# Performance work log

Measured on AMD Instinct MI355X. Metric: run time of the kernel, lower is better.

## Reference

```python
import jax, jax.numpy as jnp
import numpy as np

N, C, H, W = 64, 384, 56, 56   # local feature map
M, D = 16, 384                  # global tokens, d_model


def setup_inputs() -> dict:
    key = jax.random.key(0)
    k0, k1, k2, k3 = jax.random.split(key, 4)
    local_feature = jax.random.normal(k0, (N, C, H, W), dtype=jnp.float32)
    x = jax.random.normal(k1, (N, M, D), dtype=jnp.float32)
    # nn.Linear params: weight [out, in], bias [out]
    Wq = jax.random.normal(k2, (C, D), dtype=jnp.float32) * (1.0 / np.sqrt(D))
    bq = jnp.zeros((C,), dtype=jnp.float32)
    Wu = jax.random.normal(k3, (D, C), dtype=jnp.float32) * (1.0 / np.sqrt(C))
    bu = jnp.zeros((D,), dtype=jnp.float32)
    return {"local_feature": local_feature, "x": x, "Wq": Wq, "bq": bq, "Wu": Wu, "bu": bu}


def reference(local_feature, x, Wq, bq, Wu, bu):
    n, c, h, w = local_feature.shape
    # n c h w -> n (h w) c
    lf = local_feature.reshape(n, c, h * w).transpose(0, 2, 1)  # [n, L, c]
    q = x @ Wq.T + bq                                           # [n, M, c]
    scores = jnp.einsum('nmc,nlc->nml', q, lf) * (c ** -0.5)    # [n, M, L]
    attn = jax.nn.softmax(scores, axis=-1)
    fusion = jnp.einsum('nml,nlc->nmc', attn, lf)               # [n, M, c]
    return fusion @ Wu.T + bu + x                               # residual to x
```

## Files before the change

kernel.cpp:

```cpp
#include <hip/hip_runtime.h>
#include <math.h>

#define N_ 64
#define C_ 384
#define L_ 3136
#define M_ 16
#define D_ 384

__global__ __launch_bounds__(128) void k1_qproj(const float* __restrict__ x,
                                                const float* __restrict__ Wq,
                                                const float* __restrict__ bq,
                                                float* __restrict__ qs) {
    const int n = blockIdx.x;
    const int c = blockIdx.y * 128 + threadIdx.x;
    const float4* __restrict__ wrow = (const float4*)(Wq + (size_t)c * D_);
    const float4* __restrict__ xn   = (const float4*)(x + (size_t)n * M_ * D_);
    float acc[M_];
#pragma unroll
    for (int m = 0; m < M_; ++m) acc[m] = 0.f;
    for (int dq = 0; dq < D_ / 4; ++dq) {
        const float4 wv = wrow[dq];
#pragma unroll
        for (int m = 0; m < M_; ++m) {
            const float4 xv = xn[m * (D_ / 4) + dq];
            acc[m] += wv.x * xv.x + wv.y * xv.y + wv.z * xv.z + wv.w * xv.w;
        }
    }
    const float rs = 0.05103103630798287f;
    const float b = bq[c];
    float* qout = qs + ((size_t)n * C_ + c) * M_;
#pragma unroll
    for (int m = 0; m < M_; ++m) qout[m] = (acc[m] + b) * rs;
}

__global__ __launch_bounds__(256) void k2_scores(const float* __restrict__ lf,
                                                 const float* __restrict__ qs,
                                                 float* __restrict__ scores) {
    const int n = blockIdx.x;
    const int s = blockIdx.y;
    const int t = threadIdx.x;
    const bool active = (t < 224);
    const int l0 = s * 448 + (active ? t : 0) * 2;
    const float* __restrict__ lfn = lf + (size_t)n * C_ * L_;
    const float* __restrict__ qn  = qs + (size_t)n * C_ * M_;
    float accx[M_], accy[M_];
#pragma unroll
    for (int m = 0; m < M_; ++m) { accx[m] = 0.f; accy[m] = 0.f; }
    if (active) {
#pragma unroll 4
        for (int c = 0; c < C_; ++c) {
            const float2 lv = *(const float2*)(lfn + (size_t)c * L_ + l0);
            const float* __restrict__ qv = qn + c * M_;
#pragma unroll
            for (int m = 0; m < M_; ++m) {
                accx[m] += qv[m] * lv.x;
                accy[m] += qv[m] * lv.y;
            }
        }
        float* sn = scores + (size_t)n * M_ * L_;
#pragma unroll
        for (int m = 0; m < M_; ++m) {
            *(float2*)(sn + (size_t)m * L_ + l0) = make_float2(accx[m], accy[m]);
        }
    }
}

__global__ __launch_bounds__(64) void k3_softmax(float* __restrict__ scores) {
    float* row = scores + (size_t)blockIdx.x * L_;
    const int t = threadIdx.x;
    float lmax = -1e30f;
    for (int i = t; i < L_ / 4; i += 64) {
        const float4 v = ((const float4*)row)[i];
        lmax = fmaxf(lmax, fmaxf(fmaxf(v.x, v.y), fmaxf(v.z, v.w)));
    }
#pragma unroll
    for (int o = 32; o > 0; o >>= 1) lmax = fmaxf(lmax, __shfl_xor(lmax, o, 64));
    float lsum = 0.f;
    for (int i = t; i < L_ / 4; i += 64) {
        const float4 v = ((const float4*)row)[i];
        lsum += expf(v.x - lmax) + expf(v.y - lmax) +
                expf(v.z - lmax) + expf(v.w - lmax);
    }
#pragma unroll
    for (int o = 32; o > 0; o >>= 1) lsum += __shfl_xor(lsum, o, 64);
    const float inv = 1.0f / lsum;
    for (int i = t; i < L_ / 4; i += 64) {
        float4 v = ((const float4*)row)[i];
        v.x = expf(v.x - lmax) * inv;
        v.y = expf(v.y - lmax) * inv;
        v.z = expf(v.z - lmax) * inv;
        v.w = expf(v.w - lmax) * inv;
        ((float4*)row)[i] = v;
    }
}

__global__ __launch_bounds__(384) void k4_fusion(const float* __restrict__ lf,
                                                 const float* __restrict__ attn,
                                                 float* __restrict__ fusionP) {
    const int n = blockIdx.x;
    const int s = blockIdx.y;
    const int c = threadIdx.x;
    const float* __restrict__ lrow = lf + ((size_t)n * C_ + c) * L_;
    const float* __restrict__ an   = attn + (size_t)n * M_ * L_;
    float acc[M_];
#pragma unroll
    for (int m = 0; m < M_; ++m) acc[m] = 0.f;
    const int l0 = s * 392;
#pragma unroll 2
    for (int lq = 0; lq < 98; ++lq) {
        const int l = l0 + lq * 4;
        const float4 lv = *(const float4*)(lrow + l);
#pragma unroll
        for (int m = 0; m < M_; ++m) {
            const float4 av = *(const float4*)(an + (size_t)m * L_ + l);
            acc[m] += av.x * lv.x + av.y * lv.y + av.z * lv.z + av.w * lv.w;
        }
    }
    float* fp = fusionP + ((size_t)(n * 8 + s) * M_) * C_;
#pragma unroll
    for (int m = 0; m < M_; ++m) fp[m * C_ + c] = acc[m];
}

__global__ __launch_bounds__(256) void k4b_reduce(float* __restrict__ fusionP) {
    const int i = blockIdx.x * 256 + threadIdx.x;
    const int n = i / (M_ * C_);
    const int mc = i % (M_ * C_);
    float* p = fusionP + (size_t)n * 8 * M_ * C_ + mc;
    float v = p[0];
#pragma unroll
    for (int s2 = 1; s2 < 8; ++s2) v += p[s2 * M_ * C_];
    p[0] = v;
}

__global__ __launch_bounds__(128) void k5_out(const float* __restrict__ fusionP,
                                              const float* __restrict__ Wu,
                                              const float* __restrict__ bu,
                                              const float* __restrict__ x,
                                              float* __restrict__ out) {
    const int n = blockIdx.x;
    const int d = blockIdx.y * 128 + threadIdx.x;
    const float4* __restrict__ wrow = (const float4*)(Wu + (size_t)d * C_);
    const float4* __restrict__ fn   = (const float4*)(fusionP + (size_t)n * 8 * M_ * C_);
    float acc[M_];
#pragma unroll
    for (int m = 0; m < M_; ++m) acc[m] = 0.f;
    for (int cq = 0; cq < C_ / 4; ++cq) {
        const float4 wv = wrow[cq];
#pragma unroll
        for (int m = 0; m < M_; ++m) {
            const float4 fv = fn[m * (C_ / 4) + cq];
            acc[m] += wv.x * fv.x + wv.y * fv.y + wv.z * fv.z + wv.w * fv.w;
        }
    }
    const float b = bu[d];
#pragma unroll
    for (int m = 0; m < M_; ++m) {
        const size_t o = ((size_t)n * M_ + m) * D_ + d;
        out[o] = acc[m] + b + x[o];
    }
}

extern "C" void kernel_launch(void* const* d_in, const int* in_sizes, int n_in,
                              void* d_out, int out_size, void* d_ws, size_t ws_size,
                              hipStream_t stream) {
    const float* lf = (const float*)d_in[0];
    const float* x  = (const float*)d_in[1];
    const float* Wq = (const float*)d_in[2];
    const float* bq = (const float*)d_in[3];
    const float* Wu = (const float*)d_in[4];
    const float* bu = (const float*)d_in[5];
    float* out = (float*)d_out;

    float* ws      = (float*)d_ws;
    float* qs      = ws;
    float* scores  = qs + 393216;
    float* fusionP = scores + 3211264;

    k1_qproj  <<<dim3(64, 3), 128, 0, stream>>>(x, Wq, bq, qs);
    k2_scores <<<dim3(64, 7), 256, 0, stream>>>(lf, qs, scores);
    k3_softmax<<<1024, 64, 0, stream>>>(scores);
    k4_fusion <<<dim3(64, 8), 384, 0, stream>>>(lf, scores, fusionP);
    k4b_reduce<<<1536, 256, 0, stream>>>(fusionP);
    k5_out    <<<dim3(64, 3), 128, 0, stream>>>(fusionP, Wu, bu, x, out);
}
```

Baseline: 644.4 us.

## Fuse exp into scores, defer softmax normalization, tile fusion kernel through LDS

```diff
diff --git a/kernel.cpp b/kernel.cpp
--- a/kernel.cpp
+++ b/kernel.cpp
@@ -6,6 +6,7 @@
 #define L_ 3136
 #define M_ 16
 #define D_ 384
+#define SPL 49
 
 __global__ __launch_bounds__(128) void k1_qproj(const float* __restrict__ x,
                                                 const float* __restrict__ Wq,
@@ -33,114 +34,154 @@
     for (int m = 0; m < M_; ++m) qout[m] = (acc[m] + b) * rs;
 }
 
-__global__ __launch_bounds__(256) void k2_scores(const float* __restrict__ lf,
-                                                 const float* __restrict__ qs,
-                                                 float* __restrict__ scores) {
-    const int n = blockIdx.x;
-    const int s = blockIdx.y;
+__global__ __launch_bounds__(64) void k2_scores_exp(const float* __restrict__ lf,
+                                                    const float* __restrict__ qs,
+                                                    float* __restrict__ e_out,
+                                                    float* __restrict__ Sp) {
+    const int s = blockIdx.x;
+    const int n = blockIdx.y;
     const int t = threadIdx.x;
-    const bool active = (t < 224);
-    const int l0 = s * 448 + (active ? t : 0) * 2;
-    const float* __restrict__ lfn = lf + (size_t)n * C_ * L_;
+    const int l = s * 64 + t;
+    const float* __restrict__ lfn = lf + (size_t)n * C_ * L_ + l;
     const float* __restrict__ qn  = qs + (size_t)n * C_ * M_;
-    float accx[M_], accy[M_];
-#pragma unroll
-    for (int m = 0; m < M_; ++m) { accx[m] = 0.f; accy[m] = 0.f; }
-    if (active) {
-#pragma unroll 4
-        for (int c = 0; c < C_; ++c) {
-            const float2 lv = *(const float2*)(lfn + (size_t)c * L_ + l0);
-            const float* __restrict__ qv = qn + c * M_;
-#pragma unroll
-            for (int m = 0; m < M_; ++m) {
-                accx[m] += qv[m] * lv.x;
-                accy[m] += qv[m] * lv.y;
-            }
-        }
-        float* sn = scores + (size_t)n * M_ * L_;
-#pragma unroll
-        for (int m = 0; m < M_; ++m) {
-            *(float2*)(sn + (size_t)m * L_ + l0) = make_float2(accx[m], accy[m]);
-        }
-    }
-}
-
-__global__ __launch_bounds__(64) void k3_softmax(float* __restrict__ scores) {
-    float* row = scores + (size_t)blockIdx.x * L_;
-    const int t = threadIdx.x;
-    float lmax = -1e30f;
-    for (int i = t; i < L_ / 4; i += 64) {
-        const float4 v = ((const float4*)row)[i];
-        lmax = fmaxf(lmax, fmaxf(fmaxf(v.x, v.y), fmaxf(v.z, v.w)));
-    }
-#pragma unroll
-    for (int o = 32; o > 0; o >>= 1) lmax = fmaxf(lmax, __shfl_xor(lmax, o, 64));
-    float lsum = 0.f;
-    for (int i = t; i < L_ / 4; i += 64) {
-        const float4 v = ((const float4*)row)[i];
-        lsum += expf(v.x - lmax) + expf(v.y - lmax) +
-                expf(v.z - lmax) + expf(v.w - lmax);
-    }
-#pragma unroll
-    for (int o = 32; o > 0; o >>= 1) lsum += __shfl_xor(lsum, o, 64);
-    const float inv = 1.0f / lsum;
-    for (int i = t; i < L_ / 4; i += 64) {
-        float4 v = ((const float4*)row)[i];
-        v.x = expf(v.x - lmax) * inv;
-        v.y = expf(v.y - lmax) * inv;
-        v.z = expf(v.z - lmax) * inv;
-        v.w = expf(v.w - lmax) * inv;
-        ((float4*)row)[i] = v;
-    }
-}
-
-__global__ __launch_bounds__(384) void k4_fusion(const float* __restrict__ lf,
-                                                 const float* __restrict__ attn,
-                                                 float* __restrict__ fusionP) {
-    const int n = blockIdx.x;
-    const int s = blockIdx.y;
-    const int c = threadIdx.x;
-    const float* __restrict__ lrow = lf + ((size_t)n * C_ + c) * L_;
-    const float* __restrict__ an   = attn + (size_t)n * M_ * L_;
     float acc[M_];
 #pragma unroll
     for (int m = 0; m < M_; ++m) acc[m] = 0.f;
-    const int l0 = s * 392;
-#pragma unroll 2
-    for (int lq = 0; lq < 98; ++lq) {
-        const int l = l0 + lq * 4;
-        const float4 lv = *(const float4*)(lrow + l);
-#pragma unroll
-        for (int m = 0; m < M_; ++m) {
-            const float4 av = *(const float4*)(an + (size_t)m * L_ + l);
-            acc[m] += av.x * lv.x + av.y * lv.y + av.z * lv.z + av.w * lv.w;
-        }
-    }
-    float* fp = fusionP + ((size_t)(n * 8 + s) * M_) * C_;
-#pragma unroll
-    for (int m = 0; m < M_; ++m) fp[m * C_ + c] = acc[m];
-}
-
-__global__ __launch_bounds__(256) void k4b_reduce(float* __restrict__ fusionP) {
-    const int i = blockIdx.x * 256 + threadIdx.x;
-    const int n = i / (M_ * C_);
-    const int mc = i % (M_ * C_);
-    float* p = fusionP + (size_t)n * 8 * M_ * C_ + mc;
-    float v = p[0];
-#pragma unroll
-    for (int s2 = 1; s2 < 8; ++s2) v += p[s2 * M_ * C_];
-    p[0] = v;
-}
-
-__global__ __launch_bounds__(128) void k5_out(const float* __restrict__ fusionP,
+    for (int c = 0; c < C_; c += 8) {
+        float lv[8];
+#pragma unroll
+        for (int u = 0; u < 8; ++u) lv[u] = lfn[(size_t)(c + u) * L_];
+#pragma unroll
+        for (int u = 0; u < 8; ++u) {
+            const float lvu = lv[u];
+            const float4* __restrict__ qv = (const float4*)(qn + (size_t)(c + u) * M_);
+            const float4 q0 = qv[0], q1 = qv[1], q2 = qv[2], q3 = qv[3];
+            acc[0]  += q0.x * lvu; acc[1]  += q0.y * lvu; acc[2]  += q0.z * lvu; acc[3]  += q0.w * lvu;
+            acc[4]  += q1.x * lvu; acc[5]  += q1.y * lvu; acc[6]  += q1.z * lvu; acc[7]  += q1.w * lvu;
+            acc[8]  += q2.x * lvu; acc[9]  += q2.y * lvu; acc[10] += q2.z * lvu; acc[11] += q2.w * lvu;
+            acc[12] += q3.x * lvu; acc[13] += q3.y * lvu; acc[14] += q3.z * lvu; acc[15] += q3.w * lvu;
+        }
+    }
+    float e[M_];
+#pragma unroll
+    for (int m = 0; m < M_; ++m) e[m] = __expf(acc[m]);
+    float* __restrict__ eo = e_out + (size_t)n * M_ * L_ + l;
+#pragma unroll
+    for (int m = 0; m < M_; ++m) eo[(size_t)m * L_] = e[m];
+    float own = 0.f;
+#pragma unroll
+    for (int m = 0; m < M_; ++m) {
+        float v = e[m];
+#pragma unroll
+        for (int o = 32; o > 0; o >>= 1) v += __shfl_xor(v, o, 64);
+        if (t == m) own = v;
+    }
+    if (t < M_) Sp[((size_t)n * SPL + s) * M_ + t] = own;
+}
+
+__global__ __launch_bounds__(256) void k4_fusion(const float* __restrict__ lf,
+                                                 const float* __restrict__ e_in,
+                                                 float* __restrict__ fusion) {
+    const int cb = blockIdx.x;
+    const int n  = blockIdx.y;
+    const int u  = threadIdx.x;
+    const int c0 = cb * 32;
+    const int jg = u >> 5;
+    const int cg = (u >> 2) & 7;
+    const int mg = u & 3;
+    const int lst = u & 63;
+    const int wv  = u >> 6;
+    const int swz_w = 4 * ((lst >> 3) & 7);
+    const int swz_r = 4 * jg;
+    const int emask = (mg * 4) ^ swz_r;
+    const int cmask = (cg * 4) ^ swz_r;
+
+    __shared__ float lf_lds[64][36];
+    __shared__ float e_lds[64][36];
+    __shared__ float red[8][516];
+
+    float acc[16];
+#pragma unroll
+    for (int i = 0; i < 16; ++i) acc[i] = 0.f;
+
+    const float* __restrict__ lfb = lf + ((size_t)n * C_ + c0) * L_ + lst;
+    const float* __restrict__ eb  = e_in + (size_t)n * M_ * L_ + lst;
+
+    float plf[8], pe[4];
+#pragma unroll
+    for (int i = 0; i < 8; ++i) plf[i] = lfb[(size_t)(wv * 8 + i) * L_];
+#pragma unroll
+    for (int k = 0; k < 4; ++k) pe[k] = eb[(size_t)(wv * 4 + k) * L_];
+
+    for (int lt = 0; lt < SPL; ++lt) {
+        __syncthreads();
+        *(float4*)&lf_lds[lst][(wv * 8 + 0) ^ swz_w] = make_float4(plf[0], plf[1], plf[2], plf[3]);
+        *(float4*)&lf_lds[lst][(wv * 8 + 4) ^ swz_w] = make_float4(plf[4], plf[5], plf[6], plf[7]);
+        *(float4*)&e_lds[lst][(wv * 4) ^ swz_w]      = make_float4(pe[0], pe[1], pe[2], pe[3]);
+        if (lt + 1 < SPL) {
+            const int l0 = (lt + 1) * 64;
+#pragma unroll
+            for (int i = 0; i < 8; ++i) plf[i] = lfb[(size_t)(wv * 8 + i) * L_ + l0];
+#pragma unroll
+            for (int k = 0; k < 4; ++k) pe[k] = eb[(size_t)(wv * 4 + k) * L_ + l0];
+        }
+        __syncthreads();
+#pragma unroll
+        for (int jj = 0; jj < 8; ++jj) {
+            const int j = jg * 8 + jj;
+            const float4 ev = *(const float4*)&e_lds[j][emask];
+            const float4 lv = *(const float4*)&lf_lds[j][cmask];
+            acc[0]  += ev.x * lv.x; acc[1]  += ev.x * lv.y; acc[2]  += ev.x * lv.z; acc[3]  += ev.x * lv.w;
+            acc[4]  += ev.y * lv.x; acc[5]  += ev.y * lv.y; acc[6]  += ev.y * lv.z; acc[7]  += ev.y * lv.w;
+            acc[8]  += ev.z * lv.x; acc[9]  += ev.z * lv.y; acc[10] += ev.z * lv.z; acc[11] += ev.z * lv.w;
+            acc[12] += ev.w * lv.x; acc[13] += ev.w * lv.y; acc[14] += ev.w * lv.z; acc[15] += ev.w * lv.w;
+        }
+    }
+#pragma unroll
+    for (int mi = 0; mi < 4; ++mi) {
+        *(float4*)&red[jg][(mg * 4 + mi) * 32 + cg * 4] =
+            make_float4(acc[mi * 4 + 0], acc[mi * 4 + 1], acc[mi * 4 + 2], acc[mi * 4 + 3]);
+    }
+    __syncthreads();
+    float* __restrict__ fout = fusion + (size_t)n * M_ * C_ + c0;
+#pragma unroll
+    for (int r = 0; r < 2; ++r) {
+        const int o = u + r * 256;
+        const int m = o >> 5;
+        const int crel = o & 31;
+        float sum = 0.f;
+#pragma unroll
+        for (int g = 0; g < 8; ++g) sum += red[g][o];
+        fout[(size_t)m * C_ + crel] = sum;
+    }
+}
+
+__global__ __launch_bounds__(128) void k5_out(const float* __restrict__ fusion,
+                                              const float* __restrict__ Sp,
                                               const float* __restrict__ Wu,
                                               const float* __restrict__ bu,
                                               const float* __restrict__ x,
                                               float* __restrict__ out) {
     const int n = blockIdx.x;
     const int d = blockIdx.y * 128 + threadIdx.x;
+    float S[M_];
+#pragma unroll
+    for (int m = 0; m < M_; ++m) S[m] = 0.f;
+    const float* __restrict__ spn = Sp + (size_t)n * SPL * M_;
+    for (int s = 0; s < SPL; ++s) {
+        const float4* __restrict__ sp4 = (const float4*)(spn + s * M_);
+        const float4 a = sp4[0], b2 = sp4[1], c2 = sp4[2], d2 = sp4[3];
+        S[0]  += a.x;  S[1]  += a.y;  S[2]  += a.z;  S[3]  += a.w;
+        S[4]  += b2.x; S[5]  += b2.y; S[6]  += b2.z; S[7]  += b2.w;
+        S[8]  += c2.x; S[9]  += c2.y; S[10] += c2.z; S[11] += c2.w;
+        S[12] += d2.x; S[13] += d2.y; S[14] += d2.z; S[15] += d2.w;
+    }
+    float inv[M_];
+#pragma unroll
+    for (int m = 0; m < M_; ++m) inv[m] = 1.0f / S[m];
+
     const float4* __restrict__ wrow = (const float4*)(Wu + (size_t)d * C_);
-    const float4* __restrict__ fn   = (const float4*)(fusionP + (size_t)n * 8 * M_ * C_);
+    const float4* __restrict__ fn   = (const float4*)(fusion + (size_t)n * M_ * C_);
     float acc[M_];
 #pragma unroll
     for (int m = 0; m < M_; ++m) acc[m] = 0.f;
@@ -156,7 +197,7 @@
 #pragma unroll
     for (int m = 0; m < M_; ++m) {
         const size_t o = ((size_t)n * M_ + m) * D_ + d;
-        out[o] = acc[m] + b + x[o];
+        out[o] = acc[m] * inv[m] + b + x[o];
     }
 }
 
@@ -171,15 +212,14 @@
     const float* bu = (const float*)d_in[5];
     float* out = (float*)d_out;
 
-    float* ws      = (float*)d_ws;
-    float* qs      = ws;
-    float* scores  = qs + 393216;
-    float* fusionP = scores + 3211264;
-
-    k1_qproj  <<<dim3(64, 3), 128, 0, stream>>>(x, Wq, bq, qs);
-    k2_scores <<<dim3(64, 7), 256, 0, stream>>>(lf, qs, scores);
-    k3_softmax<<<1024, 64, 0, stream>>>(scores);
-    k4_fusion <<<dim3(64, 8), 384, 0, stream>>>(lf, scores, fusionP);
-    k4b_reduce<<<1536, 256, 0, stream>>>(fusionP);
-    k5_out    <<<dim3(64, 3), 128, 0, stream>>>(fusionP, Wu, bu, x, out);
-}
+    float* ws     = (float*)d_ws;
+    float* qs     = ws;
+    float* e      = qs + 393216;
+    float* Sp     = e + 3211264;
+    float* fusion = Sp + 64 * SPL * M_;
+
+    k1_qproj     <<<dim3(64, 3),   128, 0, stream>>>(x, Wq, bq, qs);
+    k2_scores_exp<<<dim3(SPL, 64),  64, 0, stream>>>(lf, qs, e, Sp);
+    k4_fusion    <<<dim3(12, 64),  256, 0, stream>>>(lf, e, fusion);
+    k5_out       <<<dim3(64, 3),   128, 0, stream>>>(fusion, Sp, Wu, bu, x, out);
+}
```

After: 579.5 us. -10.1%, faster.

## Fuse scores, softmax and attention-weighted sum into one streaming kernel

Applied to the files above, without the earlier changes.

```diff
diff --git a/kernel.cpp b/kernel.cpp
--- a/kernel.cpp
+++ b/kernel.cpp
@@ -6,6 +6,7 @@
 #define L_ 3136
 #define M_ 16
 #define D_ 384
+#define G_ 8
 
 __global__ __launch_bounds__(128) void k1_qproj(const float* __restrict__ x,
                                                 const float* __restrict__ Wq,
@@ -33,114 +34,186 @@
     for (int m = 0; m < M_; ++m) qout[m] = (acc[m] + b) * rs;
 }
 
-__global__ __launch_bounds__(256) void k2_scores(const float* __restrict__ lf,
+__global__ __launch_bounds__(512) void k24_fused(const float* __restrict__ lf,
                                                  const float* __restrict__ qs,
-                                                 float* __restrict__ scores) {
-    const int n = blockIdx.x;
-    const int s = blockIdx.y;
-    const int t = threadIdx.x;
-    const bool active = (t < 224);
-    const int l0 = s * 448 + (active ? t : 0) * 2;
-    const float* __restrict__ lfn = lf + (size_t)n * C_ * L_;
+                                                 float* __restrict__ fusionP,
+                                                 float* __restrict__ Sp) {
+    const int n  = blockIdx.x;
+    const int lg = blockIdx.y;
+    const int u  = threadIdx.x;
+    const int lane = u & 63;
+    const int wv   = u >> 6;
+
+    const int t0 = (lg == 0) ? 0 : (6 * lg + 1);
+    const int nt = (lg == 0) ? 7 : 6;
+
+    __shared__ float lf_lds[12][64][36];
+    __shared__ float e_lds[16][68];
+    __shared__ float red[8][16][64];
+
+    const int jg = u >> 7;
+    const int cg = ((u >> 6) & 1) * 16 + ((u >> 2) & 15);
+    const int mg = u & 3;
+    const int swz_w = 4 * ((lane >> 3) & 7);
+
+    const float* __restrict__ lfb = lf + (size_t)n * C_ * L_;
     const float* __restrict__ qn  = qs + (size_t)n * C_ * M_;
-    float accx[M_], accy[M_];
-#pragma unroll
-    for (int m = 0; m < M_; ++m) { accx[m] = 0.f; accy[m] = 0.f; }
-    if (active) {
-#pragma unroll 4
-        for (int c = 0; c < C_; ++c) {
-            const float2 lv = *(const float2*)(lfn + (size_t)c * L_ + l0);
-            const float* __restrict__ qv = qn + c * M_;
-#pragma unroll
-            for (int m = 0; m < M_; ++m) {
-                accx[m] += qv[m] * lv.x;
-                accy[m] += qv[m] * lv.y;
+
+    float accB[4][12];
+#pragma unroll
+    for (int a = 0; a < 4; ++a)
+#pragma unroll
+        for (int b = 0; b < 12; ++b) accB[a][b] = 0.f;
+
+    float val[48];
+    {
+        const int l0 = t0 * 64 + lane;
+#pragma unroll
+        for (int ch = 0; ch < 12; ++ch)
+#pragma unroll
+            for (int i = 0; i < 4; ++i)
+                val[ch * 4 + i] = lfb[(size_t)(ch * 32 + wv * 4 + i) * L_ + l0];
+    }
+    float SaccA = 0.f, SaccB = 0.f;
+
+    for (int it = 0; it < nt; ++it) {
+        float accA[16];
+#pragma unroll
+        for (int m = 0; m < 16; ++m) accA[m] = 0.f;
+#pragma unroll
+        for (int ch = 0; ch < 12; ++ch) {
+#pragma unroll
+            for (int i = 0; i < 4; ++i) {
+                const int c = ch * 32 + wv * 4 + i;
+                const float v = val[ch * 4 + i];
+                const float4* __restrict__ qv = (const float4*)(qn + (size_t)c * M_);
+                const float4 q0 = qv[0], q1 = qv[1], q2 = qv[2], q3 = qv[3];
+                accA[0]  += q0.x * v; accA[1]  += q0.y * v; accA[2]  += q0.z * v; accA[3]  += q0.w * v;
+                accA[4]  += q1.x * v; accA[5]  += q1.y * v; accA[6]  += q1.z * v; accA[7]  += q1.w * v;
+                accA[8]  += q2.x * v; accA[9]  += q2.y * v; accA[10] += q2.z * v; accA[11] += q2.w * v;
+                accA[12] += q3.x * v; accA[13] += q3.y * v; accA[14] += q3.z * v; accA[15] += q3.w * v;
             }
         }
-        float* sn = scores + (size_t)n * M_ * L_;
-#pragma unroll
-        for (int m = 0; m < M_; ++m) {
-            *(float2*)(sn + (size_t)m * L_ + l0) = make_float2(accx[m], accy[m]);
-        }
-    }
-}
-
-__global__ __launch_bounds__(64) void k3_softmax(float* __restrict__ scores) {
-    float* row = scores + (size_t)blockIdx.x * L_;
-    const int t = threadIdx.x;
-    float lmax = -1e30f;
-    for (int i = t; i < L_ / 4; i += 64) {
-        const float4 v = ((const float4*)row)[i];
-        lmax = fmaxf(lmax, fmaxf(fmaxf(v.x, v.y), fmaxf(v.z, v.w)));
-    }
-#pragma unroll
-    for (int o = 32; o > 0; o >>= 1) lmax = fmaxf(lmax, __shfl_xor(lmax, o, 64));
-    float lsum = 0.f;
-    for (int i = t; i < L_ / 4; i += 64) {
-        const float4 v = ((const float4*)row)[i];
-        lsum += expf(v.x - lmax) + expf(v.y - lmax) +
-                expf(v.z - lmax) + expf(v.w - lmax);
-    }
-#pragma unroll
-    for (int o = 32; o > 0; o >>= 1) lsum += __shfl_xor(lsum, o, 64);
-    const float inv = 1.0f / lsum;
-    for (int i = t; i < L_ / 4; i += 64) {
-        float4 v = ((const float4*)row)[i];
-        v.x = expf(v.x - lmax) * inv;
-        v.y = expf(v.y - lmax) * inv;
-        v.z = expf(v.z - lmax) * inv;
-        v.w = expf(v.w - lmax) * inv;
-        ((float4*)row)[i] = v;
-    }
-}
-
-__global__ __launch_bounds__(384) void k4_fusion(const float* __restrict__ lf,
-                                                 const float* __restrict__ attn,
-                                                 float* __restrict__ fusionP) {
-    const int n = blockIdx.x;
-    const int s = blockIdx.y;
-    const int c = threadIdx.x;
-    const float* __restrict__ lrow = lf + ((size_t)n * C_ + c) * L_;
-    const float* __restrict__ an   = attn + (size_t)n * M_ * L_;
-    float acc[M_];
-#pragma unroll
-    for (int m = 0; m < M_; ++m) acc[m] = 0.f;
-    const int l0 = s * 392;
-#pragma unroll 2
-    for (int lq = 0; lq < 98; ++lq) {
-        const int l = l0 + lq * 4;
-        const float4 lv = *(const float4*)(lrow + l);
-#pragma unroll
-        for (int m = 0; m < M_; ++m) {
-            const float4 av = *(const float4*)(an + (size_t)m * L_ + l);
-            acc[m] += av.x * lv.x + av.y * lv.y + av.z * lv.z + av.w * lv.w;
-        }
-    }
-    float* fp = fusionP + ((size_t)(n * 8 + s) * M_) * C_;
-#pragma unroll
-    for (int m = 0; m < M_; ++m) fp[m * C_ + c] = acc[m];
+#pragma unroll
+        for (int ch = 0; ch < 12; ++ch)
+            *(float4*)&lf_lds[ch][lane][(wv * 4) ^ swz_w] =
+                make_float4(val[ch * 4 + 0], val[ch * 4 + 1], val[ch * 4 + 2], val[ch * 4 + 3]);
+#pragma unroll
+        for (int m = 0; m < 16; ++m) red[wv][m][lane] = accA[m];
+        __syncthreads();
+        {
+            float s1 = 0.f, s2 = 0.f;
+#pragma unroll
+            for (int w = 0; w < 8; ++w) s1 += red[w][wv][lane];
+#pragma unroll
+            for (int w = 0; w < 8; ++w) s2 += red[w][8 + wv][lane];
+            const float e1 = __expf(s1), e2 = __expf(s2);
+            e_lds[wv][lane]     = e1;
+            e_lds[8 + wv][lane] = e2;
+            SaccA += e1;
+            SaccB += e2;
+        }
+        if (it + 1 < nt) {
+            const int l0 = (t0 + it + 1) * 64 + lane;
+#pragma unroll
+            for (int ch = 0; ch < 12; ++ch)
+#pragma unroll
+                for (int i = 0; i < 4; ++i)
+                    val[ch * 4 + i] = lfb[(size_t)(ch * 32 + wv * 4 + i) * L_ + l0];
+        }
+        __syncthreads();
+#pragma unroll
+        for (int jj = 0; jj < 16; ++jj) {
+            const int j = jg * 16 + jj;
+            const int swzj = 4 * (((jg << 1) + (jj >> 3)) & 7);
+            float es[4];
+#pragma unroll
+            for (int mi = 0; mi < 4; ++mi) es[mi] = e_lds[mg * 4 + mi][j];
+#pragma unroll
+            for (int qi = 0; qi < 3; ++qi) {
+                const float4 lv = *(const float4*)&lf_lds[(cg >> 3) + 4 * qi][j][(4 * (cg & 7)) ^ swzj];
+#pragma unroll
+                for (int mi = 0; mi < 4; ++mi) {
+                    accB[mi][qi * 4 + 0] += es[mi] * lv.x;
+                    accB[mi][qi * 4 + 1] += es[mi] * lv.y;
+                    accB[mi][qi * 4 + 2] += es[mi] * lv.z;
+                    accB[mi][qi * 4 + 3] += es[mi] * lv.w;
+                }
+            }
+        }
+        __syncthreads();
+    }
+
+    float* part = &lf_lds[0][0][0];
+#pragma unroll
+    for (int mi = 0; mi < 4; ++mi)
+#pragma unroll
+        for (int qi = 0; qi < 3; ++qi) {
+            const int m = mg * 4 + mi;
+            const int cb = 4 * cg + 128 * qi;
+            *(float4*)&part[(jg * 16 + m) * 384 + cb] =
+                make_float4(accB[mi][qi * 4 + 0], accB[mi][qi * 4 + 1],
+                            accB[mi][qi * 4 + 2], accB[mi][qi * 4 + 3]);
+        }
+    __syncthreads();
+    float* __restrict__ fout = fusionP + (size_t)(n * G_ + lg) * M_ * C_;
+#pragma unroll
+    for (int k = 0; k < 12; ++k) {
+        const int o = u + 512 * k;
+        const int m = o / 384;
+        const int c = o % 384;
+        const float s = part[(0 * 16 + m) * 384 + c] + part[(1 * 16 + m) * 384 + c] +
+                        part[(2 * 16 + m) * 384 + c] + part[(3 * 16 + m) * 384 + c];
+        fout[o] = s;
+    }
+    float sa = SaccA, sb = SaccB;
+#pragma unroll
+    for (int o = 32; o > 0; o >>= 1) { sa += __shfl_xor(sa, o, 64); sb += __shfl_xor(sb, o, 64); }
+    if (lane == 0) {
+        float* spn = Sp + (size_t)(n * G_ + lg) * M_;
+        spn[wv]     = sa;
+        spn[8 + wv] = sb;
+    }
 }
 
 __global__ __launch_bounds__(256) void k4b_reduce(float* __restrict__ fusionP) {
     const int i = blockIdx.x * 256 + threadIdx.x;
     const int n = i / (M_ * C_);
     const int mc = i % (M_ * C_);
-    float* p = fusionP + (size_t)n * 8 * M_ * C_ + mc;
+    float* p = fusionP + (size_t)n * G_ * M_ * C_ + mc;
     float v = p[0];
 #pragma unroll
-    for (int s2 = 1; s2 < 8; ++s2) v += p[s2 * M_ * C_];
+    for (int s2 = 1; s2 < G_; ++s2) v += p[s2 * M_ * C_];
     p[0] = v;
 }
 
 __global__ __launch_bounds__(128) void k5_out(const float* __restrict__ fusionP,
+                                              const float* __restrict__ Sp,
                                               const float* __restrict__ Wu,
                                               const float* __restrict__ bu,
                                               const float* __restrict__ x,
                                               float* __restrict__ out) {
     const int n = blockIdx.x;
     const int d = blockIdx.y * 128 + threadIdx.x;
+    float S[M_];
+#pragma unroll
+    for (int m = 0; m < M_; ++m) S[m] = 0.f;
+    const float* __restrict__ spn = Sp + (size_t)n * G_ * M_;
+#pragma unroll
+    for (int s = 0; s < G_; ++s) {
+        const float4* __restrict__ sp4 = (const float4*)(spn + s * M_);
+        const float4 a = sp4[0], b2 = sp4[1], c2 = sp4[2], d2 = sp4[3];
+        S[0]  += a.x;  S[1]  += a.y;  S[2]  += a.z;  S[3]  += a.w;
+        S[4]  += b2.x; S[5]  += b2.y; S[6]  += b2.z; S[7]  += b2.w;
+        S[8]  += c2.x; S[9]  += c2.y; S[10] += c2.z; S[11] += c2.w;
+        S[12] += d2.x; S[13] += d2.y; S[14] += d2.z; S[15] += d2.w;
+    }
+    float inv[M_];
+#pragma unroll
+    for (int m = 0; m < M_; ++m) inv[m] = 1.0f / S[m];
+
     const float4* __restrict__ wrow = (const float4*)(Wu + (size_t)d * C_);
-    const float4* __restrict__ fn   = (const float4*)(fusionP + (size_t)n * 8 * M_ * C_);
+    const float4* __restrict__ fn   = (const float4*)(fusionP + (size_t)n * G_ * M_ * C_);
     float acc[M_];
 #pragma unroll
     for (int m = 0; m < M_; ++m) acc[m] = 0.f;
@@ -156,7 +229,7 @@
 #pragma unroll
     for (int m = 0; m < M_; ++m) {
         const size_t o = ((size_t)n * M_ + m) * D_ + d;
-        out[o] = acc[m] + b + x[o];
+        out[o] = acc[m] * inv[m] + b + x[o];
     }
 }
 
@@ -173,13 +246,11 @@
 
     float* ws      = (float*)d_ws;
     float* qs      = ws;
-    float* scores  = qs + 393216;
-    float* fusionP = scores + 3211264;
-
-    k1_qproj  <<<dim3(64, 3), 128, 0, stream>>>(x, Wq, bq, qs);
-    k2_scores <<<dim3(64, 7), 256, 0, stream>>>(lf, qs, scores);
-    k3_softmax<<<1024, 64, 0, stream>>>(scores);
-    k4_fusion <<<dim3(64, 8), 384, 0, stream>>>(lf, scores, fusionP);
+    float* fusionP = qs + 393216;
+    float* Sp      = fusionP + 3145728;
+
+    k1_qproj <<<dim3(64, 3), 128, 0, stream>>>(x, Wq, bq, qs);
+    k24_fused<<<dim3(64, G_), 512, 0, stream>>>(lf, qs, fusionP, Sp);
     k4b_reduce<<<1536, 256, 0, stream>>>(fusionP);
-    k5_out    <<<dim3(64, 3), 128, 0, stream>>>(fusionP, Wu, bu, x, out);
-}
+    k5_out   <<<dim3(64, 3), 128, 0, stream>>>(fusionP, Sp, Wu, bu, x, out);
+}
```

New measurement: 2.207 ms. 243% more time.
